# Kernel tuning notes

Measured on AMD Instinct MI355X. Metric: run time of the kernel, lower is better.

Reference implementation:

```python
import jax, jax.numpy as jnp
import numpy as np

N_NODES = 100000
N_EDGES = 1600000
N_QUERY = 500000
F_IN, HID, EMB = 7, 128, 64


def _glorot(key, fan_in, fan_out):
    lim = float(np.sqrt(6.0 / (fan_in + fan_out)))
    return jax.random.uniform(key, (fan_in, fan_out), jnp.float32, -lim, lim)


def setup_inputs() -> dict:
    key = jax.random.key(0)
    ks = jax.random.split(key, 16)
    x = jax.random.normal(ks[0], (N_NODES, F_IN), jnp.float32)
    edge_index = jax.random.randint(ks[1], (2, N_EDGES), 0, N_NODES, jnp.int64)
    query_edges = jax.random.randint(ks[2], (2, N_QUERY), 0, N_NODES, jnp.int64)
    return {
        "x": x,
        "edge_index": edge_index,
        "query_edges": query_edges,
        # GCN layer 1 / 2
        "W1": _glorot(ks[3], F_IN, HID), "b1": jnp.zeros((HID,), jnp.float32),
        "W2": _glorot(ks[4], HID, HID), "b2": jnp.zeros((HID,), jnp.float32),
        # encoder fc
        "Wfc": _glorot(ks[5], HID, EMB), "bfc": jnp.zeros((EMB,), jnp.float32),
        # decoder MLP
        "Wd1": _glorot(ks[6], 2 * EMB, HID), "bd1": jnp.zeros((HID,), jnp.float32),
        "Wd2": _glorot(ks[7], HID, HID // 2), "bd2": jnp.zeros((HID // 2,), jnp.float32),
        "Wd3": _glorot(ks[8], HID // 2, 1), "bd3": jnp.zeros((1,), jnp.float32),
    }


def _gcn_conv(x, W, b, src, dst, n_nodes):
    """PyG GCNConv: add self-loops + symmetric deg^{-1/2} normalization."""
    h = x @ W  # [N, F_out]
    deg = jnp.ones((n_nodes,), h.dtype).at[dst].add(jnp.ones_like(dst, h.dtype))  # +1 self-loop
    dinv = jax.lax.rsqrt(deg)
    norm = dinv[src] * dinv[dst]  # [E]
    agg = jnp.zeros_like(h).at[dst].add(h[src] * norm[:, None])  # scatter-add messages
    agg = agg + h * (dinv * dinv)[:, None]  # self-loop contribution
    return agg + b


def reference(x, edge_index, query_edges, W1, b1, W2, b2, Wfc, bfc, Wd1, bd1, Wd2, bd2, Wd3, bd3):
    n = x.shape[0]
    src, dst = edge_index[0], edge_index[1]
    # encoder (eval mode: dropout = identity)
    h = jax.nn.relu(_gcn_conv(x, W1, b1, src, dst, n))
    h = jax.nn.relu(_gcn_conv(h, W2, b2, src, dst, n))
    z = h @ Wfc + bfc  # [N, EMB]
    # pair gather + MLP decode
    zc = jnp.concatenate([z[query_edges[0]], z[query_edges[1]]], axis=-1)  # [Q, 2*EMB]
    d = jax.nn.relu(zc @ Wd1 + bd1)
    d = jax.nn.relu(d @ Wd2 + bd2)
    logits = (d @ Wd3 + bd3).squeeze(-1)  # [Q]
    return jax.nn.sigmoid(logits)
```

## Files before the change

### kernel.cpp

```cpp
#include <hip/hip_runtime.h>
#include <hip/hip_bf16.h>
#include <cstdint>
#include <cstddef>

constexpr int TPB = 256;
constexpr int SCAN_B = 1024;
constexpr int NB   = 128;
constexpr int BSH  = 10;
constexpr int NPB  = 1 << BSH;
constexpr int EPB  = 4096;
using bf16x8 = __attribute__((ext_vector_type(8))) short;
using f32x4  = __attribute__((ext_vector_type(4))) float;

static inline int cdiv(int a, int b) { return (a + b - 1) / b; }

__device__ __forceinline__ float bf2f(short u) {
  return __uint_as_float(((unsigned int)(unsigned short)u) << 16);
}
__device__ __forceinline__ short f2bf(float f) {
  unsigned int u = __float_as_uint(f);
  return (short)((u + 0x7FFF + ((u >> 16) & 1)) >> 16);
}


__global__ __launch_bounds__(256)
void bucket_hist_kernel(const int* __restrict__ dst, int* __restrict__ bh,
                        int e_cnt, int n_blk) {
  __shared__ int h[NB];
  int tid = threadIdx.x;
  if (tid < NB) h[tid] = 0;
  __syncthreads();
  int base = blockIdx.x * EPB;
  for (int i = tid; i < EPB; i += TPB) {
    int e = base + i;
    if (e < e_cnt) atomicAdd(&h[dst[e] >> BSH], 1);
  }
  __syncthreads();
  if (tid < NB) bh[tid * n_blk + blockIdx.x] = h[tid];
}

__global__ __launch_bounds__(SCAN_B)
void scan_block_kernel(const int* __restrict__ counts, int* __restrict__ rowptr,
                       int* __restrict__ bsum, int n) {
  __shared__ int wsum[16];
  const int tid = threadIdx.x;
  const int i = blockIdx.x * SCAN_B + tid;
  const int lane = tid & 63;
  const int w = tid >> 6;
  int v = (i < n) ? counts[i] : 0;
  int s = v;
  #pragma unroll
  for (int off = 1; off < 64; off <<= 1) {
    int t = __shfl_up(s, off, 64);
    if (lane >= off) s += t;
  }
  if (lane == 63) wsum[w] = s;
  __syncthreads();
  if (tid < 16) {
    int ws_ = wsum[tid];
    #pragma unroll
    for (int off = 1; off < 16; off <<= 1) {
      int t = __shfl_up(ws_, off, 64);
      if (tid >= off) ws_ += t;
    }
    wsum[tid] = ws_;
  }
  __syncthreads();
  int woff = (w == 0) ? 0 : wsum[w - 1];
  if (i < n) rowptr[i] = woff + s - v;
  if (tid == SCAN_B - 1) bsum[blockIdx.x] = woff + s;
}

__global__ void scan_carry_kernel(int* bsum, int nb) {
  __shared__ int w0;
  int tid = threadIdx.x;
  int v = (tid < nb) ? bsum[tid] : 0;
  int s = v;
  #pragma unroll
  for (int off = 1; off < 64; off <<= 1) {
    int t = __shfl_up(s, off, 64);
    if ((tid & 63) >= off) s += t;
  }
  if (tid == 63) w0 = s;
  __syncthreads();
  int incl = s + ((tid >= 64) ? w0 : 0);
  if (tid < nb) bsum[tid] = incl - v;
}

__global__ void scan_add_kernel(int* rowptr, const int* __restrict__ bsum, int n, int total) {
  int i = blockIdx.x * TPB + threadIdx.x;
  if (i < n) rowptr[i] += bsum[i / SCAN_B];
  if (i == 0) rowptr[n] = total;
}

__global__ __launch_bounds__(256)
void bucket_scatter_kernel(const int* __restrict__ src, const int* __restrict__ dst,
                           const int* __restrict__ eoff, unsigned int* __restrict__ ebuf,
                           int e_cnt, int n_blk) {
  __shared__ int cur[NB];
  int tid = threadIdx.x;
  if (tid < NB) cur[tid] = eoff[tid * n_blk + blockIdx.x];
  __syncthreads();
  int base = blockIdx.x * EPB;
  for (int i = tid; i < EPB; i += TPB) {
    int e = base + i;
    if (e < e_cnt) {
      int d = dst[e];
      int b = d >> BSH;
      int pos = atomicAdd(&cur[b], 1);
      ebuf[pos] = ((unsigned int)src[e] << BSH) | (unsigned int)(d & (NPB - 1));
    }
  }
}

__global__ __launch_bounds__(256)
void node_hist_kernel(const unsigned int* __restrict__ ebuf, const int* __restrict__ eoff,
                      int* __restrict__ counts, int n_blk, int n_nodes) {
  __shared__ int nh[NPB];
  int b = blockIdx.x;
  for (int i = threadIdx.x; i < NPB; i += TPB) nh[i] = 0;
  __syncthreads();
  int wb = eoff[b * n_blk];
  int we = eoff[(b + 1) * n_blk];
  for (int i = wb + threadIdx.x; i < we; i += TPB)
    atomicAdd(&nh[ebuf[i] & (NPB - 1)], 1);
  __syncthreads();
  int nbase = b << BSH;
  for (int i = threadIdx.x; i < NPB; i += TPB) {
    int node = nbase + i;
    if (node < n_nodes) counts[node] = nh[i];
  }
}

__global__ void dinv_kernel(const int* __restrict__ counts, float* dinv, int n) {
  int i = blockIdx.x * TPB + threadIdx.x;
  if (i < n) dinv[i] = rsqrtf((float)counts[i] + 1.0f);
}

__global__ __launch_bounds__(256)
void final_scatter_kernel(const unsigned int* __restrict__ ebuf, const int* __restrict__ eoff,
                          const int* __restrict__ rowptr, int* __restrict__ csr_src,
                          int n_blk, int n_nodes) {
  __shared__ int cur[NPB];
  int b = blockIdx.x;
  int nbase = b << BSH;
  for (int i = threadIdx.x; i < NPB; i += TPB) {
    int node = nbase + i;
    cur[i] = (node < n_nodes) ? rowptr[node] : 0;
  }
  __syncthreads();
  int wb = eoff[b * n_blk];
  int we = eoff[(b + 1) * n_blk];
  for (int i = wb + threadIdx.x; i < we; i += TPB) {
    unsigned int p = ebuf[i];
    int pos = atomicAdd(&cur[p & (NPB - 1)], 1);
    csr_src[pos] = (int)(p >> BSH);
  }
}


__global__ void pad_x8_kernel(const float* __restrict__ x, float* __restrict__ x8, int n) {
  int i = blockIdx.x * TPB + threadIdx.x;
  if (i >= n * 8) return;
  int node = i >> 3, f = i & 7;
  x8[i] = (f < 7) ? x[node * 7 + f] : 0.0f;
}

__global__ void pad_w1_kernel(const float* __restrict__ W1, float* __restrict__ W1p) {
  int i = blockIdx.x * TPB + threadIdx.x;
  if (i < 8 * 128) W1p[i] = (i < 7 * 128) ? W1[i] : 0.0f;
}

__global__ void wconv_kernel(const float* __restrict__ in, unsigned short* __restrict__ out,
                             int K, int N) {
  int i = blockIdx.x * TPB + threadIdx.x;
  if (i >= K * N) return;
  int k = i / N, n = i - k * N;
  out[(size_t)n * K + k] = (unsigned short)f2bf(in[i]);
}

__global__ __launch_bounds__(256)
void agg_x_kernel(const int* __restrict__ rowptr, const int* __restrict__ csr_src,
                  const float* __restrict__ dinv, const float* __restrict__ x8,
                  float* __restrict__ aggx, int n_nodes) {
  int gid = blockIdx.x * TPB + threadIdx.x;
  int node = gid >> 3;
  int f = gid & 7;
  if (node >= n_nodes) return;
  float dn = dinv[node];
  float acc = x8[(size_t)node * 8 + f] * dn * dn;
  int beg = rowptr[node], end = rowptr[node + 1];
  for (int i = beg; i < end; ++i) {
    int s = csr_src[i];
    acc = fmaf(x8[(size_t)s * 8 + f], dinv[s] * dn, acc);
  }
  aggx[(size_t)node * 8 + f] = acc;
}

__global__ __launch_bounds__(256)
void gather4_kernel(const int* __restrict__ rowptr, const int* __restrict__ csr_src,
                    const float* __restrict__ dinv, const uint4* __restrict__ h1s,
                    uint4* __restrict__ g1, int n_nodes) {
  int wid = (blockIdx.x * TPB + threadIdx.x) >> 6;
  if (wid >= n_nodes) return;
  int lane = threadIdx.x & 63;
  int qtr = lane >> 4;
  int l = lane & 15;
  float acc[8];
  #pragma unroll
  for (int j = 0; j < 8; ++j) acc[j] = 0.0f;
  auto addv = [&](uint4 v) {
    unsigned int u[4] = {v.x, v.y, v.z, v.w};
    #pragma unroll
    for (int p = 0; p < 4; ++p) {
      acc[2 * p]     += __uint_as_float(u[p] << 16);
      acc[2 * p + 1] += __uint_as_float(u[p] & 0xffff0000u);
    }
  };
  if (qtr == 0) addv(h1s[(size_t)wid * 16 + l]);
  int beg = rowptr[wid], end = rowptr[wid + 1];
  int i = beg + qtr;
  for (; i + 4 < end; i += 8) {
    int s0 = csr_src[i];
    int s1 = csr_src[i + 4];
    uint4 v0 = h1s[(size_t)s0 * 16 + l];
    uint4 v1 = h1s[(size_t)s1 * 16 + l];
    addv(v0);
    addv(v1);
  }
  if (i < end) addv(h1s[(size_t)csr_src[i] * 16 + l]);
  #pragma unroll
  for (int j = 0; j < 8; ++j) {
    acc[j] += __shfl_xor(acc[j], 16, 64);
    acc[j] += __shfl_xor(acc[j], 32, 64);
  }
  if (qtr == 0) {
    float dn = dinv[wid];
    unsigned int w[4];
    #pragma unroll
    for (int p = 0; p < 4; ++p) {
      unsigned int lo = (unsigned int)(unsigned short)f2bf(acc[2 * p] * dn);
      unsigned int hi = (unsigned int)(unsigned short)f2bf(acc[2 * p + 1] * dn);
      w[p] = lo | (hi << 16);
    }
    uint4 o; o.x = w[0]; o.y = w[1]; o.z = w[2]; o.w = w[3];
    g1[(size_t)wid * 16 + l] = o;
  }
}

template<int K, int CO, bool OB, bool SC>
__global__ __launch_bounds__(256)
void mm_tiled(const float* __restrict__ in, const float* __restrict__ W,
              const float* __restrict__ bias, const float* __restrict__ scale,
              void* __restrict__ outv, int n_rows, int do_relu) {
  constexpr int BM = 64;
  constexpr int BK = (K % 32 == 0) ? 32 : K;
  constexpr int SS = BK + 1 + (BK & 1);
  constexpr int TM = 4;
  constexpr int TN = CO / 16;
  __shared__ float s_in[BM][SS];
  __shared__ float s_w[BK][CO];
  const int tid = threadIdx.x;
  const int base = blockIdx.x * BM;
  const int tr = tid >> 4;
  const int tc = tid & 15;

  float acc[TM][TN];
  #pragma unroll
  for (int m = 0; m < TM; ++m)
    #pragma unroll
    for (int n = 0; n < TN; ++n) acc[m][n] = 0.0f;

  for (int kb = 0; kb < K; kb += BK) {
    if constexpr (BK % 4 == 0) {
      constexpr int F4 = BM * (BK / 4);
      #pragma unroll
      for (int t = tid; t < F4; t += TPB) {
        int r = t / (BK / 4), c4 = t % (BK / 4);
        int row = base + r;
        float4 v = make_float4(0.f, 0.f, 0.f, 0.f);
        if (row < n_rows) v = *(const float4*)(in + (size_t)row * K + kb + c4 * 4);
        s_in[r][c4 * 4 + 0] = v.x;
        s_in[r][c4 * 4 + 1] = v.y;
        s_in[r][c4 * 4 + 2] = v.z;
        s_in[r][c4 * 4 + 3] = v.w;
      }
    } else {
      for (int t = tid; t < BM * BK; t += TPB) {
        int r = t / BK, c = t % BK;
        int row = base + r;
        s_in[r][c] = (row < n_rows) ? in[(size_t)row * K + kb + c] : 0.0f;
      }
    }
    {
      constexpr int WF4 = BK * CO / 4;
      #pragma unroll
      for (int t = tid; t < WF4; t += TPB)
        *(float4*)(&s_w[0][0] + t * 4) = *(const float4*)(W + (size_t)kb * CO + t * 4);
    }
    __syncthreads();

    #pragma unroll
    for (int kk = 0; kk < BK; ++kk) {
      float a[TM], b[TN];
      #pragma unroll
      for (int m = 0; m < TM; ++m) a[m] = s_in[tr * TM + m][kk];
      #pragma unroll
      for (int n = 0; n < TN; ++n) b[n] = s_w[kk][tc + 16 * n];
      #pragma unroll
      for (int m = 0; m < TM; ++m)
        #pragma unroll
        for (int n = 0; n < TN; ++n) acc[m][n] = fmaf(a[m], b[n], acc[m][n]);
    }
    __syncthreads();
  }

  #pragma unroll
  for (int m = 0; m < TM; ++m) {
    int row = base + tr * TM + m;
    if (row < n_rows) {
      float sc = 1.0f;
      if constexpr (SC) sc = scale[row];
      #pragma unroll
      for (int n = 0; n < TN; ++n) {
        int j = tc + 16 * n;
        float v = acc[m][n] + (bias ? bias[j] : 0.0f);
        if (do_relu) v = fmaxf(v, 0.0f);
        if constexpr (SC) v *= sc;
        if constexpr (OB)
          ((unsigned short*)outv)[(size_t)row * CO + j] = (unsigned short)f2bf(v);
        else
          ((float*)outv)[(size_t)row * CO + j] = v;
      }
    }
  }
}

template<int K, int N>
__global__ __launch_bounds__(256)
void mm_mfma(const unsigned short* __restrict__ A, const unsigned short* __restrict__ WT,
             const float* __restrict__ bias, unsigned short* __restrict__ out,
             int n_rows, int do_relu) {
  constexpr int KS = K / 32;
  constexpr int NT = N / 16;
  const int lane = threadIdx.x & 63;
  const int col = lane & 15;
  const int sub = lane >> 4;
  const int wid = threadIdx.x >> 6;

  bf16x8 bfrag[KS][NT];
  #pragma unroll
  for (int ks = 0; ks < KS; ++ks)
    #pragma unroll
    for (int nt = 0; nt < NT; ++nt)
      bfrag[ks][nt] = *(const bf16x8*)(WT + (size_t)(nt * 16 + col) * K + ks * 32 + sub * 8);
  float bv[NT];
  #pragma unroll
  for (int nt = 0; nt < NT; ++nt) bv[nt] = bias ? bias[nt * 16 + col] : 0.0f;

  int ntiles = (n_rows + 15) >> 4;
  int stride = gridDim.x * 4;
  for (int tile = blockIdx.x * 4 + wid; tile < ntiles; tile += stride) {
    int row_a = tile * 16 + col;
    if (row_a >= n_rows) row_a = n_rows - 1;
    bf16x8 afrag[KS];
    #pragma unroll
    for (int ks = 0; ks < KS; ++ks)
      afrag[ks] = *(const bf16x8*)(A + (size_t)row_a * K + ks * 32 + sub * 8);
    f32x4 acc[NT];
    #pragma unroll
    for (int nt = 0; nt < NT; ++nt) acc[nt] = {0.f, 0.f, 0.f, 0.f};
    #pragma unroll
    for (int ks = 0; ks < KS; ++ks)
      #pragma unroll
      for (int nt = 0; nt < NT; ++nt)
        acc[nt] = __builtin_amdgcn_mfma_f32_16x16x32_bf16(afrag[ks], bfrag[ks][nt], acc[nt], 0, 0, 0);
    #pragma unroll
    for (int r = 0; r < 4; ++r) {
      int ro = tile * 16 + sub * 4 + r;
      if (ro < n_rows) {
        #pragma unroll
        for (int nt = 0; nt < NT; ++nt) {
          float v = acc[nt][r] + bv[nt];
          if (do_relu) v = fmaxf(v, 0.0f);
          out[(size_t)ro * N + nt * 16 + col] = (unsigned short)f2bf(v);
        }
      }
    }
  }
}

__global__ __launch_bounds__(256)
void decoder_mfma_kernel(const int* __restrict__ qsrc, const int* __restrict__ qdst,
                         const unsigned short* __restrict__ atab,
                         const unsigned short* __restrict__ btab,
                         const float* __restrict__ Wd2, const float* __restrict__ bd2,
                         const float* __restrict__ Wd3, const float* __restrict__ bd3,
                         float* __restrict__ out, int n_query) {
  const int lane = threadIdx.x & 63;
  const int col = lane & 15;
  const int sub = lane >> 4;

  bf16x8 bfrag[4][4];
  #pragma unroll
  for (int ks = 0; ks < 4; ++ks)
    #pragma unroll
    for (int nt = 0; nt < 4; ++nt) {
      bf16x8 f;
      #pragma unroll
      for (int j = 0; j < 8; ++j) {
        int k = ks * 32 + sub * 8 + j;
        int n = nt * 16 + col;
        f[j] = f2bf(Wd2[k * 64 + n]);
      }
      bfrag[ks][nt] = f;
    }
  float bd2v[4], wd3v[4];
  #pragma unroll
  for (int nt = 0; nt < 4; ++nt) {
    bd2v[nt] = bd2[nt * 16 + col];
    wd3v[nt] = Wd3[nt * 16 + col];
  }
  const float bd3s = bd3[0];

  int wave = (blockIdx.x * TPB + threadIdx.x) >> 6;
  int nwaves = gridDim.x * (TPB / 64);
  int ntiles = (n_query + 15) >> 4;
  for (int t = wave; t < ntiles; t += nwaves) {
    int qb = t << 4;
    int q = qb + col;
    if (q >= n_query) q = n_query - 1;
    int si = qsrc[q], di = qdst[q];
    const bf16x8* ar = (const bf16x8*)(atab + (size_t)si * 128);
    const bf16x8* br = (const bf16x8*)(btab + (size_t)di * 128);
    bf16x8 afrag[4];
    #pragma unroll
    for (int ks = 0; ks < 4; ++ks) {
      bf16x8 av = ar[ks * 4 + sub];
      bf16x8 bv = br[ks * 4 + sub];
      bf16x8 d;
      #pragma unroll
      for (int j = 0; j < 8; ++j)
        d[j] = f2bf(fmaxf(bf2f(av[j]) + bf2f(bv[j]), 0.0f));
      afrag[ks] = d;
    }
    f32x4 acc[4];
    #pragma unroll
    for (int nt = 0; nt < 4; ++nt) acc[nt] = {0.f, 0.f, 0.f, 0.f};
    #pragma unroll
    for (int ks = 0; ks < 4; ++ks)
      #pragma unroll
      for (int nt = 0; nt < 4; ++nt)
        acc[nt] = __builtin_amdgcn_mfma_f32_16x16x32_bf16(afrag[ks], bfrag[ks][nt], acc[nt], 0, 0, 0);
    float part[4] = {0.f, 0.f, 0.f, 0.f};
    #pragma unroll
    for (int nt = 0; nt < 4; ++nt)
      #pragma unroll
      for (int r = 0; r < 4; ++r) {
        float v = fmaxf(acc[nt][r] + bd2v[nt], 0.0f);
        part[r] = fmaf(v, wd3v[nt], part[r]);
      }
    #pragma unroll
    for (int off = 1; off < 16; off <<= 1)
      #pragma unroll
      for (int r = 0; r < 4; ++r) part[r] += __shfl_xor(part[r], off, 64);
    if (col == 0) {
      int row0 = qb + sub * 4;
      #pragma unroll
      for (int r = 0; r < 4; ++r) {
        int qq = row0 + r;
        if (qq < n_query) out[qq] = 1.0f / (1.0f + __expf(-(part[r] + bd3s)));
      }
    }
  }
}

extern "C" void kernel_launch(void* const* d_in, const int* in_sizes, int n_in,
                              void* d_out, int out_size, void* d_ws, size_t ws_size,
                              hipStream_t stream) {
  const float* x    = (const float*)d_in[0];
  const int*   ei   = (const int*)d_in[1];
  const int*   qe   = (const int*)d_in[2];
  const float* W1   = (const float*)d_in[3];
  const float* b1   = (const float*)d_in[4];
  const float* W2   = (const float*)d_in[5];
  const float* b2   = (const float*)d_in[6];
  const float* Wfc  = (const float*)d_in[7];
  const float* bfc  = (const float*)d_in[8];
  const float* Wd1  = (const float*)d_in[9];
  const float* bd1  = (const float*)d_in[10];
  const float* Wd2  = (const float*)d_in[11];
  const float* bd2  = (const float*)d_in[12];
  const float* Wd3  = (const float*)d_in[13];
  const float* bd3  = (const float*)d_in[14];
  float* out = (float*)d_out;

  const int n_nodes = in_sizes[0] / 7;
  const int n_edges = in_sizes[1] / 2;
  const int n_query = in_sizes[2] / 2;
  const int* e_src = ei;
  const int* e_dst = ei + n_edges;
  const int* q_src = qe;
  const int* q_dst = qe + n_query;

  const int n_blk1 = cdiv(n_edges, EPB);
  const int bh_len = NB * n_blk1;
  const int n_bucket = cdiv(n_nodes, NPB);

  char* wp = (char*)d_ws;
  auto take = [&](size_t bytes) { char* p = wp; wp += (bytes + 255) & ~size_t(255); return p; };
  float* dinv    = (float*)take((size_t)n_nodes * 4);
  int*   counts  = (int*)  take((size_t)n_nodes * 4);
  int*   rowptr  = (int*)  take((size_t)(n_nodes + 1) * 4);
  int*   bsum    = (int*)  take(512 * 4);
  int*   bh      = (int*)  take((size_t)(bh_len + 1) * 4);
  int*   eoff    = (int*)  take((size_t)(bh_len + 1) * 4);
  unsigned int* ebuf = (unsigned int*)take((size_t)n_edges * 4);
  int*   csr_src = (int*)  take((size_t)n_edges * 4);
  float* x8      = (float*)take((size_t)n_nodes * 8 * 4);
  float* aggx    = (float*)take((size_t)n_nodes * 8 * 4);
  float* W1p     = (float*)take(8 * 128 * 4);
  unsigned short* W2T   = (unsigned short*)take(128 * 128 * 2);
  unsigned short* WfcT  = (unsigned short*)take(64 * 128 * 2);
  unsigned short* Wd1aT = (unsigned short*)take(128 * 64 * 2);
  unsigned short* Wd1bT = (unsigned short*)take(128 * 64 * 2);
  float* bufP    = (float*)take((size_t)n_nodes * 128 * 4);
  float* bufQ    = (float*)take((size_t)n_nodes * 128 * 4);
  float* bufR    = (float*)take((size_t)n_nodes * 64 * 4);

  const int mm_blocks = cdiv(n_nodes, 64);
  const int node_blocks = cdiv(n_nodes, TPB);
  const int scan_blocks = cdiv(n_nodes, SCAN_B);
  const int escan_blocks = cdiv(bh_len, SCAN_B);
  const int mfma_blocks = min(1024, cdiv(cdiv(n_nodes, 16), 4));

  bucket_hist_kernel<<<n_blk1, TPB, 0, stream>>>(e_dst, bh, n_edges, n_blk1);
  scan_block_kernel<<<escan_blocks, SCAN_B, 0, stream>>>(bh, eoff, bsum, bh_len);
  scan_carry_kernel<<<1, 128, 0, stream>>>(bsum, escan_blocks);
  scan_add_kernel<<<cdiv(bh_len, TPB), TPB, 0, stream>>>(eoff, bsum, bh_len, n_edges);
  bucket_scatter_kernel<<<n_blk1, TPB, 0, stream>>>(e_src, e_dst, eoff, ebuf, n_edges, n_blk1);
  node_hist_kernel<<<n_bucket, TPB, 0, stream>>>(ebuf, eoff, counts, n_blk1, n_nodes);
  dinv_kernel<<<node_blocks, TPB, 0, stream>>>(counts, dinv, n_nodes);
  scan_block_kernel<<<scan_blocks, SCAN_B, 0, stream>>>(counts, rowptr, bsum, n_nodes);
  scan_carry_kernel<<<1, 128, 0, stream>>>(bsum, scan_blocks);
  scan_add_kernel<<<node_blocks, TPB, 0, stream>>>(rowptr, bsum, n_nodes, n_edges);
  final_scatter_kernel<<<n_bucket, TPB, 0, stream>>>(ebuf, eoff, rowptr, csr_src, n_blk1, n_nodes);

  pad_x8_kernel<<<cdiv(n_nodes * 8, TPB), TPB, 0, stream>>>(x, x8, n_nodes);
  pad_w1_kernel<<<4, TPB, 0, stream>>>(W1, W1p);
  wconv_kernel<<<cdiv(128 * 128, TPB), TPB, 0, stream>>>(W2, W2T, 128, 128);
  wconv_kernel<<<cdiv(128 * 64, TPB), TPB, 0, stream>>>(Wfc, WfcT, 128, 64);
  wconv_kernel<<<cdiv(64 * 128, TPB), TPB, 0, stream>>>(Wd1, Wd1aT, 64, 128);
  wconv_kernel<<<cdiv(64 * 128, TPB), TPB, 0, stream>>>(Wd1 + 64 * 128, Wd1bT, 64, 128);

  agg_x_kernel<<<cdiv(n_nodes * 8, TPB), TPB, 0, stream>>>(rowptr, csr_src, dinv, x8, aggx, n_nodes);
  mm_tiled<8, 128, true, true><<<mm_blocks, TPB, 0, stream>>>(aggx, W1p, b1, dinv, bufP, n_nodes, 1);

  gather4_kernel<<<cdiv(n_nodes * 64, TPB), TPB, 0, stream>>>(rowptr, csr_src, dinv,
                                                              (const uint4*)bufP, (uint4*)bufQ, n_nodes);
  mm_mfma<128, 128><<<mfma_blocks, TPB, 0, stream>>>((const unsigned short*)bufQ, W2T, b2,
                                                     (unsigned short*)bufP, n_nodes, 1);

  mm_mfma<128, 64><<<mfma_blocks, TPB, 0, stream>>>((const unsigned short*)bufP, WfcT, bfc,
                                                    (unsigned short*)bufR, n_nodes, 0);

  unsigned short* atab = (unsigned short*)bufQ;
  unsigned short* btab = (unsigned short*)bufP;
  mm_mfma<64, 128><<<mfma_blocks, TPB, 0, stream>>>((const unsigned short*)bufR, Wd1aT, bd1,
                                                    atab, n_nodes, 0);
  mm_mfma<64, 128><<<mfma_blocks, TPB, 0, stream>>>((const unsigned short*)bufR, Wd1bT, nullptr,
                                                    btab, n_nodes, 0);

  decoder_mfma_kernel<<<2048, TPB, 0, stream>>>(q_src, q_dst, atab, btab, Wd2, bd2, Wd3, bd3, out, n_query);
}
```

Measured before the change: 319.6 us.

## Fold encoder fc into decoder first layer and merge small prep kernels

Precomputes combined weights Wfc·Wd1a and Wfc·Wd1b, plus folded biases, on device. This removes the separate z = h@Wfc matmul and its intermediate buffer, so the node tables are produced directly from h with K=128 instead of K=64. It also merges the scan carry and add kernels into one, folds dinv into node_hist, packs all weight prep into a single kernel, and unrolls agg_x by two edges. Rounding to bf16 now happens on the combined weight rather than on z, which slightly changes numerics.

```diff
diff --git a/kernel.cpp b/kernel.cpp
--- a/kernel.cpp
+++ b/kernel.cpp
@@ -71,25 +71,18 @@
   if (tid == SCAN_B - 1) bsum[blockIdx.x] = woff + s;
 }
 
-__global__ void scan_carry_kernel(int* bsum, int nb) {
-  __shared__ int w0;
+__global__ __launch_bounds__(256)
+void scan_fin_kernel(int* __restrict__ rowptr, const int* __restrict__ bsum,
+                     int nb, int n, int total) {
+  __shared__ int sb[128];
   int tid = threadIdx.x;
-  int v = (tid < nb) ? bsum[tid] : 0;
-  int s = v;
-  #pragma unroll
-  for (int off = 1; off < 64; off <<= 1) {
-    int t = __shfl_up(s, off, 64);
-    if ((tid & 63) >= off) s += t;
-  }
-  if (tid == 63) w0 = s;
-  __syncthreads();
-  int incl = s + ((tid >= 64) ? w0 : 0);
-  if (tid < nb) bsum[tid] = incl - v;
-}
-
-__global__ void scan_add_kernel(int* rowptr, const int* __restrict__ bsum, int n, int total) {
-  int i = blockIdx.x * TPB + threadIdx.x;
-  if (i < n) rowptr[i] += bsum[i / SCAN_B];
+  if (tid == 0) {
+    int run = 0;
+    for (int b = 0; b < nb; ++b) { sb[b] = run; run += bsum[b]; }
+  }
+  __syncthreads();
+  int i = blockIdx.x * TPB + tid;
+  if (i < n) rowptr[i] += sb[i / SCAN_B];
   if (i == 0) rowptr[n] = total;
 }
 
@@ -115,7 +108,8 @@
 
 __global__ __launch_bounds__(256)
 void node_hist_kernel(const unsigned int* __restrict__ ebuf, const int* __restrict__ eoff,
-                      int* __restrict__ counts, int n_blk, int n_nodes) {
+                      int* __restrict__ counts, float* __restrict__ dinv,
+                      int n_blk, int n_nodes) {
   __shared__ int nh[NPB];
   int b = blockIdx.x;
   for (int i = threadIdx.x; i < NPB; i += TPB) nh[i] = 0;
@@ -128,13 +122,11 @@
   int nbase = b << BSH;
   for (int i = threadIdx.x; i < NPB; i += TPB) {
     int node = nbase + i;
-    if (node < n_nodes) counts[node] = nh[i];
-  }
-}
-
-__global__ void dinv_kernel(const int* __restrict__ counts, float* dinv, int n) {
-  int i = blockIdx.x * TPB + threadIdx.x;
-  if (i < n) dinv[i] = rsqrtf((float)counts[i] + 1.0f);
+    if (node < n_nodes) {
+      counts[node] = nh[i];
+      dinv[node] = rsqrtf((float)nh[i] + 1.0f);
+    }
+  }
 }
 
 __global__ __launch_bounds__(256)
@@ -166,18 +158,44 @@
   x8[i] = (f < 7) ? x[node * 7 + f] : 0.0f;
 }
 
-__global__ void pad_w1_kernel(const float* __restrict__ W1, float* __restrict__ W1p) {
-  int i = blockIdx.x * TPB + threadIdx.x;
-  if (i < 8 * 128) W1p[i] = (i < 7 * 128) ? W1[i] : 0.0f;
-}
-
-__global__ void wconv_kernel(const float* __restrict__ in, unsigned short* __restrict__ out,
-                             int K, int N) {
-  int i = blockIdx.x * TPB + threadIdx.x;
-  if (i >= K * N) return;
-  int k = i / N, n = i - k * N;
-  out[(size_t)n * K + k] = (unsigned short)f2bf(in[i]);
-}
+__global__ __launch_bounds__(256)
+void prep_weights_kernel(const float* __restrict__ W1, const float* __restrict__ W2,
+                         const float* __restrict__ Wfc, const float* __restrict__ bfc,
+                         const float* __restrict__ Wd1, const float* __restrict__ bd1,
+                         float* __restrict__ W1p, unsigned short* __restrict__ W2T,
+                         unsigned short* __restrict__ WcaT, unsigned short* __restrict__ WcbT,
+                         float* __restrict__ bca, float* __restrict__ bcb) {
+  int b = blockIdx.x;
+  int tid = threadIdx.x;
+  if (b == 0) {
+    for (int i = tid; i < 8 * 128; i += TPB)
+      W1p[i] = (i < 7 * 128) ? W1[i] : 0.0f;
+    int j = tid & 127;
+    int which = tid >> 7;
+    float acc = which ? 0.0f : bd1[j];
+    int mo = which ? 64 : 0;
+    #pragma unroll 8
+    for (int m = 0; m < 64; ++m) acc = fmaf(bfc[m], Wd1[(mo + m) * 128 + j], acc);
+    if (which) bcb[j] = acc; else bca[j] = acc;
+  } else if (b <= 64) {
+    int idx = (b - 1) * 256 + tid;
+    int n = idx >> 7, k = idx & 127;
+    W2T[idx] = (unsigned short)f2bf(W2[k * 128 + n]);
+  } else {
+    int idx = (b - 65) * 256 + tid;
+    int j = idx >> 7, k = idx & 127;
+    float accA = 0.0f, accB = 0.0f;
+    #pragma unroll 8
+    for (int m = 0; m < 64; ++m) {
+      float w = Wfc[k * 64 + m];
+      accA = fmaf(w, Wd1[m * 128 + j], accA);
+      accB = fmaf(w, Wd1[(64 + m) * 128 + j], accB);
+    }
+    WcaT[j * 128 + k] = (unsigned short)f2bf(accA);
+    WcbT[j * 128 + k] = (unsigned short)f2bf(accB);
+  }
+}
+
 
 __global__ __launch_bounds__(256)
 void agg_x_kernel(const int* __restrict__ rowptr, const int* __restrict__ csr_src,
@@ -188,13 +206,23 @@
   int f = gid & 7;
   if (node >= n_nodes) return;
   float dn = dinv[node];
-  float acc = x8[(size_t)node * 8 + f] * dn * dn;
+  float acc0 = x8[(size_t)node * 8 + f] * dn * dn;
+  float acc1 = 0.0f;
   int beg = rowptr[node], end = rowptr[node + 1];
-  for (int i = beg; i < end; ++i) {
+  int i = beg;
+  for (; i + 1 < end; i += 2) {
+    int s0 = csr_src[i];
+    int s1 = csr_src[i + 1];
+    float w0 = dinv[s0] * dn;
+    float w1 = dinv[s1] * dn;
+    acc0 = fmaf(x8[(size_t)s0 * 8 + f], w0, acc0);
+    acc1 = fmaf(x8[(size_t)s1 * 8 + f], w1, acc1);
+  }
+  if (i < end) {
     int s = csr_src[i];
-    acc = fmaf(x8[(size_t)s * 8 + f], dinv[s] * dn, acc);
-  }
-  aggx[(size_t)node * 8 + f] = acc;
+    acc0 = fmaf(x8[(size_t)s * 8 + f], dinv[s] * dn, acc0);
+  }
+  aggx[(size_t)node * 8 + f] = acc0 + acc1;
 }
 
 __global__ __launch_bounds__(256)
@@ -248,13 +276,13 @@
   }
 }
 
-template<int K, int CO, bool OB, bool SC>
+template<int K, int CO>
 __global__ __launch_bounds__(256)
 void mm_tiled(const float* __restrict__ in, const float* __restrict__ W,
               const float* __restrict__ bias, const float* __restrict__ scale,
-              void* __restrict__ outv, int n_rows, int do_relu) {
+              unsigned short* __restrict__ outv, int n_rows) {
   constexpr int BM = 64;
-  constexpr int BK = (K % 32 == 0) ? 32 : K;
+  constexpr int BK = K;
   constexpr int SS = BK + 1 + (BK & 1);
   constexpr int TM = 4;
   constexpr int TN = CO / 16;
@@ -271,66 +299,49 @@
     #pragma unroll
     for (int n = 0; n < TN; ++n) acc[m][n] = 0.0f;
 
-  for (int kb = 0; kb < K; kb += BK) {
-    if constexpr (BK % 4 == 0) {
-      constexpr int F4 = BM * (BK / 4);
-      #pragma unroll
-      for (int t = tid; t < F4; t += TPB) {
-        int r = t / (BK / 4), c4 = t % (BK / 4);
-        int row = base + r;
-        float4 v = make_float4(0.f, 0.f, 0.f, 0.f);
-        if (row < n_rows) v = *(const float4*)(in + (size_t)row * K + kb + c4 * 4);
-        s_in[r][c4 * 4 + 0] = v.x;
-        s_in[r][c4 * 4 + 1] = v.y;
-        s_in[r][c4 * 4 + 2] = v.z;
-        s_in[r][c4 * 4 + 3] = v.w;
-      }
-    } else {
-      for (int t = tid; t < BM * BK; t += TPB) {
-        int r = t / BK, c = t % BK;
-        int row = base + r;
-        s_in[r][c] = (row < n_rows) ? in[(size_t)row * K + kb + c] : 0.0f;
-      }
-    }
-    {
-      constexpr int WF4 = BK * CO / 4;
-      #pragma unroll
-      for (int t = tid; t < WF4; t += TPB)
-        *(float4*)(&s_w[0][0] + t * 4) = *(const float4*)(W + (size_t)kb * CO + t * 4);
-    }
-    __syncthreads();
-
-    #pragma unroll
-    for (int kk = 0; kk < BK; ++kk) {
-      float a[TM], b[TN];
-      #pragma unroll
-      for (int m = 0; m < TM; ++m) a[m] = s_in[tr * TM + m][kk];
-      #pragma unroll
-      for (int n = 0; n < TN; ++n) b[n] = s_w[kk][tc + 16 * n];
-      #pragma unroll
-      for (int m = 0; m < TM; ++m)
-        #pragma unroll
-        for (int n = 0; n < TN; ++n) acc[m][n] = fmaf(a[m], b[n], acc[m][n]);
-    }
-    __syncthreads();
+  {
+    constexpr int F4 = BM * (BK / 4);
+    #pragma unroll
+    for (int t = tid; t < F4; t += TPB) {
+      int r = t / (BK / 4), c4 = t % (BK / 4);
+      int row = base + r;
+      float4 v = make_float4(0.f, 0.f, 0.f, 0.f);
+      if (row < n_rows) v = *(const float4*)(in + (size_t)row * K + c4 * 4);
+      s_in[r][c4 * 4 + 0] = v.x;
+      s_in[r][c4 * 4 + 1] = v.y;
+      s_in[r][c4 * 4 + 2] = v.z;
+      s_in[r][c4 * 4 + 3] = v.w;
+    }
+    constexpr int WF4 = BK * CO / 4;
+    #pragma unroll
+    for (int t = tid; t < WF4; t += TPB)
+      *(float4*)(&s_w[0][0] + t * 4) = *(const float4*)(W + t * 4);
+  }
+  __syncthreads();
+
+  #pragma unroll
+  for (int kk = 0; kk < BK; ++kk) {
+    float a[TM], b[TN];
+    #pragma unroll
+    for (int m = 0; m < TM; ++m) a[m] = s_in[tr * TM + m][kk];
+    #pragma unroll
+    for (int n = 0; n < TN; ++n) b[n] = s_w[kk][tc + 16 * n];
+    #pragma unroll
+    for (int m = 0; m < TM; ++m)
+      #pragma unroll
+      for (int n = 0; n < TN; ++n) acc[m][n] = fmaf(a[m], b[n], acc[m][n]);
   }
 
   #pragma unroll
   for (int m = 0; m < TM; ++m) {
     int row = base + tr * TM + m;
     if (row < n_rows) {
-      float sc = 1.0f;
-      if constexpr (SC) sc = scale[row];
+      float sc = scale[row];
       #pragma unroll
       for (int n = 0; n < TN; ++n) {
         int j = tc + 16 * n;
-        float v = acc[m][n] + (bias ? bias[j] : 0.0f);
-        if (do_relu) v = fmaxf(v, 0.0f);
-        if constexpr (SC) v *= sc;
-        if constexpr (OB)
-          ((unsigned short*)outv)[(size_t)row * CO + j] = (unsigned short)f2bf(v);
-        else
-          ((float*)outv)[(size_t)row * CO + j] = v;
+        float v = fmaxf(acc[m][n] + bias[j], 0.0f) * sc;
+        outv[(size_t)row * CO + j] = (unsigned short)f2bf(v);
       }
     }
   }
@@ -521,9 +532,10 @@
   float* aggx    = (float*)take((size_t)n_nodes * 8 * 4);
   float* W1p     = (float*)take(8 * 128 * 4);
   unsigned short* W2T   = (unsigned short*)take(128 * 128 * 2);
-  unsigned short* WfcT  = (unsigned short*)take(64 * 128 * 2);
-  unsigned short* Wd1aT = (unsigned short*)take(128 * 64 * 2);
-  unsigned short* Wd1bT = (unsigned short*)take(128 * 64 * 2);
+  unsigned short* WcaT  = (unsigned short*)take(128 * 128 * 2);
+  unsigned short* WcbT  = (unsigned short*)take(128 * 128 * 2);
+  float* bca     = (float*)take(128 * 4);
+  float* bcb     = (float*)take(128 * 4);
   float* bufP    = (float*)take((size_t)n_nodes * 128 * 4);
   float* bufQ    = (float*)take((size_t)n_nodes * 128 * 4);
   float* bufR    = (float*)take((size_t)n_nodes * 64 * 4);
@@ -536,40 +548,31 @@
 
   bucket_hist_kernel<<<n_blk1, TPB, 0, stream>>>(e_dst, bh, n_edges, n_blk1);
   scan_block_kernel<<<escan_blocks, SCAN_B, 0, stream>>>(bh, eoff, bsum, bh_len);
-  scan_carry_kernel<<<1, 128, 0, stream>>>(bsum, escan_blocks);
-  scan_add_kernel<<<cdiv(bh_len, TPB), TPB, 0, stream>>>(eoff, bsum, bh_len, n_edges);
+  scan_fin_kernel<<<cdiv(bh_len, TPB), TPB, 0, stream>>>(eoff, bsum, escan_blocks, bh_len, n_edges);
   bucket_scatter_kernel<<<n_blk1, TPB, 0, stream>>>(e_src, e_dst, eoff, ebuf, n_edges, n_blk1);
-  node_hist_kernel<<<n_bucket, TPB, 0, stream>>>(ebuf, eoff, counts, n_blk1, n_nodes);
-  dinv_kernel<<<node_blocks, TPB, 0, stream>>>(counts, dinv, n_nodes);
+  node_hist_kernel<<<n_bucket, TPB, 0, stream>>>(ebuf, eoff, counts, dinv, n_blk1, n_nodes);
   scan_block_kernel<<<scan_blocks, SCAN_B, 0, stream>>>(counts, rowptr, bsum, n_nodes);
-  scan_carry_kernel<<<1, 128, 0, stream>>>(bsum, scan_blocks);
-  scan_add_kernel<<<node_blocks, TPB, 0, stream>>>(rowptr, bsum, n_nodes, n_edges);
+  scan_fin_kernel<<<node_blocks, TPB, 0, stream>>>(rowptr, bsum, scan_blocks, n_nodes, n_edges);
   final_scatter_kernel<<<n_bucket, TPB, 0, stream>>>(ebuf, eoff, rowptr, csr_src, n_blk1, n_nodes);
 
   pad_x8_kernel<<<cdiv(n_nodes * 8, TPB), TPB, 0, stream>>>(x, x8, n_nodes);
-  pad_w1_kernel<<<4, TPB, 0, stream>>>(W1, W1p);
-  wconv_kernel<<<cdiv(128 * 128, TPB), TPB, 0, stream>>>(W2, W2T, 128, 128);
-  wconv_kernel<<<cdiv(128 * 64, TPB), TPB, 0, stream>>>(Wfc, WfcT, 128, 64);
-  wconv_kernel<<<cdiv(64 * 128, TPB), TPB, 0, stream>>>(Wd1, Wd1aT, 64, 128);
-  wconv_kernel<<<cdiv(64 * 128, TPB), TPB, 0, stream>>>(Wd1 + 64 * 128, Wd1bT, 64, 128);
+  prep_weights_kernel<<<129, TPB, 0, stream>>>(W1, W2, Wfc, bfc, Wd1, bd1,
+                                               W1p, W2T, WcaT, WcbT, bca, bcb);
 
   agg_x_kernel<<<cdiv(n_nodes * 8, TPB), TPB, 0, stream>>>(rowptr, csr_src, dinv, x8, aggx, n_nodes);
-  mm_tiled<8, 128, true, true><<<mm_blocks, TPB, 0, stream>>>(aggx, W1p, b1, dinv, bufP, n_nodes, 1);
+  mm_tiled<8, 128><<<mm_blocks, TPB, 0, stream>>>(aggx, W1p, b1, dinv, (unsigned short*)bufP, n_nodes);
 
   gather4_kernel<<<cdiv(n_nodes * 64, TPB), TPB, 0, stream>>>(rowptr, csr_src, dinv,
                                                               (const uint4*)bufP, (uint4*)bufQ, n_nodes);
   mm_mfma<128, 128><<<mfma_blocks, TPB, 0, stream>>>((const unsigned short*)bufQ, W2T, b2,
                                                      (unsigned short*)bufP, n_nodes, 1);
 
-  mm_mfma<128, 64><<<mfma_blocks, TPB, 0, stream>>>((const unsigned short*)bufP, WfcT, bfc,
-                                                    (unsigned short*)bufR, n_nodes, 0);
-
   unsigned short* atab = (unsigned short*)bufQ;
-  unsigned short* btab = (unsigned short*)bufP;
-  mm_mfma<64, 128><<<mfma_blocks, TPB, 0, stream>>>((const unsigned short*)bufR, Wd1aT, bd1,
-                                                    atab, n_nodes, 0);
-  mm_mfma<64, 128><<<mfma_blocks, TPB, 0, stream>>>((const unsigned short*)bufR, Wd1bT, nullptr,
-                                                    btab, n_nodes, 0);
+  unsigned short* btab = (unsigned short*)bufR;
+  mm_mfma<128, 128><<<mfma_blocks, TPB, 0, stream>>>((const unsigned short*)bufP, WcaT, bca,
+                                                     atab, n_nodes, 0);
+  mm_mfma<128, 128><<<mfma_blocks, TPB, 0, stream>>>((const unsigned short*)bufP, WcbT, bcb,
+                                                     btab, n_nodes, 0);
 
   decoder_mfma_kernel<<<2048, TPB, 0, stream>>>(q_src, q_dst, atab, btab, Wd2, bd2, Wd3, bd3, out, n_query);
 }
```

Result: faster. 306.0 us (-4.2%).
